# Kernel optimization log

Hardware: AMD Instinct MI355X
Metric: run time of the kernel (lower is better)

The kernel has to match this reference:

```python
import jax, jax.numpy as jnp
import numpy as np

B, T, F_DIM = 32, 512, 128
HID, OUT, KS = 256, 4, 3
PAD_LEN = 512          # round(T * (200/stage_timepoints - 1)), stage_timepoints = 100
MMD_SIGMA = 1.0
DILATIONS = (1, 2, 4)  # config.dilation_expand = 2, num_layers = 3


def setup_inputs() -> dict:
    key = jax.random.key(0)
    keys = iter(jax.random.split(key, 40))
    s = 0.05

    def lin(o, i):
        return jax.random.normal(next(keys), (o, i), jnp.float32) * s

    def vec(o):
        return jnp.zeros((o,), jnp.float32)

    inp = {
        "feature1": jax.random.normal(next(keys), (B, F_DIM, 1, T), jnp.float32),
        "feature2": jax.random.normal(next(keys), (B, F_DIM, 1, T), jnp.float32),
    }
    # cross-attention params (A and B branches)
    for tag in ("a", "b"):
        for nm in ("q", "k", "v"):
            inp["w%s_%s" % (nm, tag)] = lin(F_DIM, F_DIM)
            inp["b%s_%s" % (nm, tag)] = vec(F_DIM)
    # TCN layers
    in_ch = F_DIM
    for i in range(3):
        inp["conv_w%d" % i] = jax.random.normal(next(keys), (HID, in_ch, KS), jnp.float32) * s
        inp["conv_b%d" % i] = vec(HID)
        inp["res_w%d" % i] = lin(HID, in_ch)
        inp["res_b%d" % i] = vec(HID)
        in_ch = HID
    inp["fc_w"] = lin(OUT, HID)
    inp["fc_b"] = vec(OUT)
    return inp


def _cross_attention(A, Bseq, wq, bq, wk, bk, wv, bv):
    # A, Bseq: [B, T, F]
    Q = A @ wq.T + bq
    K = Bseq @ wk.T + bk
    V = Bseq @ wv.T + bv
    scale = 1.0 / jnp.sqrt(jnp.asarray(Q.shape[-1], Q.dtype))
    scores = jnp.einsum('btf,bsf->bts', Q, K) * scale
    w = jax.nn.softmax(scores, axis=-1)
    return jnp.einsum('bts,bsf->btf', w, V)


def _tcn_layer(x, cw, cb, rw, rb, dilation):
    # x: [B, C, T]; causal left pad then dilated conv
    pad = (KS - 1) * dilation
    xp = jnp.pad(x, ((0, 0), (0, 0), (pad, 0)))
    out = jax.lax.conv_general_dilated(
        xp, cw, window_strides=(1,), padding='VALID',
        rhs_dilation=(dilation,), dimension_numbers=('NCH', 'OIH', 'NCH'))
    out = jax.nn.relu(out + cb[None, :, None])
    res = jnp.einsum('bct,oc->bot', x, rw) + rb[None, :, None]
    return out + res


def _pairwise_dist(x, y):
    # x, y: [B, T, F] -> [B, B, T]; ||x_i - y_j||^2 per time point via norm expansion
    sx = jnp.sum(x * x, axis=-1)  # [B, T]
    sy = jnp.sum(y * y, axis=-1)  # [B, T]
    return sx[:, None, :] + sy[None, :, :] - 2.0 * jnp.einsum('itf,jtf->ijt', x, y)


def _mmd_loss(f1, f2):
    inv = 1.0 / (2.0 * MMD_SIGMA ** 2)
    K_XX = jnp.exp(-_pairwise_dist(f1, f1) * inv)
    K_YY = jnp.exp(-_pairwise_dist(f2, f2) * inv)
    K_XY = jnp.exp(-_pairwise_dist(f1, f2) * inv)
    return jnp.mean(K_XX + K_YY - 2.0 * K_XY)


def reference(feature1, feature2,
              wq_a, bq_a, wk_a, bk_a, wv_a, bv_a,
              wq_b, bq_b, wk_b, bk_b, wv_b, bv_b,
              conv_w0, conv_b0, res_w0, res_b0,
              conv_w1, conv_b1, res_w1, res_b1,
              conv_w2, conv_b2, res_w2, res_b2,
              fc_w, fc_b):
    # [B, F, 1, T] -> [B, T, F]
    f1 = jnp.transpose(feature1[:, :, 0, :], (0, 2, 1))
    f2 = jnp.transpose(feature2[:, :, 0, :], (0, 2, 1))

    f1 = _cross_attention(f2, f1, wq_a, bq_a, wk_a, bk_a, wv_a, bv_a) * f1 + f1
    f2 = _cross_attention(f1, f2, wq_b, bq_b, wk_b, bk_b, wv_b, bv_b) * f2 + f2

    # temporal-offset padding: f1 padded right, f2 padded left, then summed
    p1 = jnp.pad(f1, ((0, 0), (0, PAD_LEN), (0, 0)))
    p2 = jnp.pad(f2, ((0, 0), (PAD_LEN, 0), (0, 0)))
    x = jnp.transpose(p1 + p2, (0, 2, 1))  # [B, F, T+PAD]

    tcn_params = ((conv_w0, conv_b0, res_w0, res_b0),
                  (conv_w1, conv_b1, res_w1, res_b1),
                  (conv_w2, conv_b2, res_w2, res_b2))
    for (cw, cb, rw, rb), d in zip(tcn_params, DILATIONS):
        x = _tcn_layer(x, cw, cb, rw, rb, d)

    pooled = jnp.mean(x, axis=2)          # [B, HID]
    output = pooled @ fc_w.T + fc_b       # [B, OUT]
    loss = _mmd_loss(f1, f2)
    return output, loss
```

## Files before the change

kernel.cpp:

```cpp
#include <hip/hip_runtime.h>

#define BB 32
#define TT 512
#define FF 128
#define HID 256
#define TP 1024

typedef __attribute__((ext_vector_type(8))) short s16x8;
typedef __attribute__((ext_vector_type(8))) unsigned short u16x8;
typedef __attribute__((ext_vector_type(4))) unsigned short u16x4;
typedef __attribute__((ext_vector_type(4))) float f32x4;

static __device__ __forceinline__ unsigned short f2bf(float f) {
    unsigned u = __builtin_bit_cast(unsigned, f);
    u = (u + 0x7FFFu + ((u >> 16) & 1u)) >> 16;
    return (unsigned short)u;
}
static __device__ __forceinline__ float bf2f(unsigned short b) {
    return __builtin_bit_cast(float, ((unsigned)b) << 16);
}

static __device__ __forceinline__ void tcnw_prep(
    int idx, const float* __restrict__ cw, const float* __restrict__ rw,
    unsigned short* __restrict__ out, int Cin)
{
    int p = idx / (256 * Cin);
    int rem = idx - p * 256 * Cin;
    int o = rem / Cin, c = rem - o * Cin;
    float v = (p < 3) ? cw[(o * Cin + c) * 3 + p] : rw[o * Cin + c];
    out[idx] = f2bf(v);
}

__global__ __launch_bounds__(256) void prep_all_kernel(
    const float* __restrict__ wqa, const float* __restrict__ wka,
    const float* __restrict__ wva, const float* __restrict__ wqb,
    const float* __restrict__ wkb, const float* __restrict__ wvb,
    const float* __restrict__ cw0, const float* __restrict__ rw0,
    const float* __restrict__ cw1, const float* __restrict__ rw1,
    const float* __restrict__ cw2, const float* __restrict__ rw2,
    unsigned short* __restrict__ qkvw, unsigned short* __restrict__ wb0,
    unsigned short* __restrict__ wb1, unsigned short* __restrict__ wb2)
{
    int idx = blockIdx.x * 256 + threadIdx.x;
    if (idx < 98304) {
        int p = idx >> 14, rc = idx & 16383;
        const float* srcs[6] = {wqa, wka, wva, wqb, wkb, wvb};
        float v = srcs[p][rc];
        if (p == 0 || p == 3) v *= 0.088388347648318447f;
        qkvw[idx] = f2bf(v);
    } else if (idx < 229376) {
        tcnw_prep(idx - 98304, cw0, rw0, wb0, 128);
    } else if (idx < 491520) {
        tcnw_prep(idx - 229376, cw1, rw1, wb1, 256);
    } else if (idx < 753664) {
        tcnw_prep(idx - 491520, cw2, rw2, wb2, 256);
    }
}

__global__ __launch_bounds__(256) void proj_mfma_kernel(
    const void* __restrict__ xq_src, int xq_mode, long long xq_bs,
    const void* __restrict__ xkv_src, int xkv_mode, long long xkv_bs,
    const unsigned short* __restrict__ w3,
    const float* __restrict__ bq, const float* __restrict__ bk,
    const float* __restrict__ bv,
    unsigned short* __restrict__ Qo, unsigned short* __restrict__ Ko,
    unsigned short* __restrict__ Vt)
{
    int t0 = blockIdx.x * 32, b = blockIdx.y;
    __shared__ __align__(16) unsigned short xsq[32 * 136];
    __shared__ __align__(16) unsigned short xskv[32 * 136];
    int tid = threadIdx.x;
    int wid = tid >> 6, lane = tid & 63;
    int n = lane & 15, g = lane >> 4;
    int tsub = (wid & 1) * 16, fh = (wid >> 1) * 64;

    if (xq_mode == 0) {
        const float* s = (const float*)xq_src + (size_t)b * xq_bs;
        for (int l = tid; l < 4096; l += 256) {
            int c = l >> 5, tt = l & 31;
            xsq[tt * 136 + c] = f2bf(s[(size_t)c * TT + t0 + tt]);
        }
    } else {
        const unsigned short* s = (const unsigned short*)xq_src + (size_t)b * xq_bs;
        for (int l = tid; l < 512; l += 256) {
            int r = l >> 4, cc = l & 15;
            *(u16x8*)&xsq[r * 136 + cc * 8] = *(const u16x8*)&s[(size_t)(t0 + r) * FF + cc * 8];
        }
    }
    if (xkv_mode == 0) {
        const float* s = (const float*)xkv_src + (size_t)b * xkv_bs;
        for (int l = tid; l < 4096; l += 256) {
            int c = l >> 5, tt = l & 31;
            xskv[tt * 136 + c] = f2bf(s[(size_t)c * TT + t0 + tt]);
        }
    } else {
        const unsigned short* s = (const unsigned short*)xkv_src + (size_t)b * xkv_bs;
        for (int l = tid; l < 512; l += 256) {
            int r = l >> 4, cc = l & 15;
            *(u16x8*)&xskv[r * 136 + cc * 8] = *(const u16x8*)&s[(size_t)(t0 + r) * FF + cc * 8];
        }
    }
    __syncthreads();

    f32x4 acc[3][4];
#pragma unroll
    for (int p = 0; p < 3; ++p)
#pragma unroll
        for (int i = 0; i < 4; ++i) acc[p][i] = (f32x4){0.f, 0.f, 0.f, 0.f};

#pragma unroll
    for (int kk = 0; kk < 4; ++kk) {
        s16x8 bxq = *(const s16x8*)&xsq[(tsub + n) * 136 + kk * 32 + g * 8];
        s16x8 bxkv = *(const s16x8*)&xskv[(tsub + n) * 136 + kk * 32 + g * 8];
#pragma unroll
        for (int i = 0; i < 4; ++i) {
            const unsigned short* wb = &w3[(size_t)(fh + i * 16 + n) * 128 + kk * 32 + g * 8];
            s16x8 a0 = *(const s16x8*)&wb[0];
            s16x8 a1 = *(const s16x8*)&wb[16384];
            s16x8 a2 = *(const s16x8*)&wb[32768];
            acc[0][i] = __builtin_amdgcn_mfma_f32_16x16x32_bf16(a0, bxq, acc[0][i], 0, 0, 0);
            acc[1][i] = __builtin_amdgcn_mfma_f32_16x16x32_bf16(a1, bxkv, acc[1][i], 0, 0, 0);
            acc[2][i] = __builtin_amdgcn_mfma_f32_16x16x32_bf16(a2, bxkv, acc[2][i], 0, 0, 0);
        }
    }

    const float scale = 0.088388347648318447f;
    int t = t0 + tsub + n;
#pragma unroll
    for (int i = 0; i < 4; ++i) {
        int fb = fh + i * 16 + g * 4;
        u16x4 pk;
#pragma unroll
        for (int r = 0; r < 4; ++r) pk[r] = f2bf(acc[0][i][r] + bq[fb + r] * scale);
        *(u16x4*)&Qo[((size_t)b * TT + t) * FF + fb] = pk;
#pragma unroll
        for (int r = 0; r < 4; ++r) pk[r] = f2bf(acc[1][i][r] + bk[fb + r]);
        *(u16x4*)&Ko[((size_t)b * TT + t) * FF + fb] = pk;
#pragma unroll
        for (int r = 0; r < 4; ++r)
            Vt[((size_t)b * FF + fb + r) * TT + t] = f2bf(acc[2][i][r] + bv[fb + r]);
    }
}

__global__ __launch_bounds__(256) void attn_mfma_kernel(
    const unsigned short* __restrict__ Qb, const unsigned short* __restrict__ Kb,
    const unsigned short* __restrict__ Vtb,
    const float* __restrict__ orig, long long bso, int cso, int tso,
    float* __restrict__ out_tf, unsigned short* __restrict__ out_x, int xoff)
{
    __shared__ __align__(16) unsigned short Ks[64 * 136];
    __shared__ __align__(16) unsigned short Vs[128 * 72];
    __shared__ __align__(16) unsigned short Ps[4 * 16 * 68];

    int t0 = blockIdx.x * 64, b = blockIdx.y;
    int tid = threadIdx.x;
    int wid = tid >> 6, lane = tid & 63;
    int n = lane & 15, g = lane >> 4;
    int q0 = t0 + wid * 16;
    unsigned short* Pw = &Ps[wid * 1088];

    s16x8 qf[4];
#pragma unroll
    for (int kk = 0; kk < 4; ++kk)
        qf[kk] = *(const s16x8*)&Qb[((size_t)b * TT + q0 + n) * FF + kk * 32 + g * 8];

    u16x8 kst[4], vst[4];
#pragma unroll
    for (int ii = 0; ii < 4; ++ii) {
        int l = tid + 256 * ii;
        kst[ii] = *(const u16x8*)&Kb[((size_t)b * TT + (l >> 4)) * FF + (l & 15) * 8];
        vst[ii] = *(const u16x8*)&Vtb[((size_t)b * FF + (l >> 3)) * TT + (l & 7) * 8];
    }

    f32x4 O[8];
#pragma unroll
    for (int ft = 0; ft < 8; ++ft) O[ft] = (f32x4){0.f, 0.f, 0.f, 0.f};
    float m[4] = {-1e30f, -1e30f, -1e30f, -1e30f};
    float lsum[4] = {0.f, 0.f, 0.f, 0.f};

    for (int it = 0; it < 8; ++it) {
        __syncthreads();
#pragma unroll
        for (int ii = 0; ii < 4; ++ii) {
            int l = tid + 256 * ii;
            *(u16x8*)&Ks[(l >> 4) * 136 + (l & 15) * 8] = kst[ii];
            *(u16x8*)&Vs[(l >> 3) * 72 + (l & 7) * 8] = vst[ii];
        }
        __syncthreads();
        if (it < 7) {
            int s0n = (it + 1) * 64;
#pragma unroll
            for (int ii = 0; ii < 4; ++ii) {
                int l = tid + 256 * ii;
                kst[ii] = *(const u16x8*)&Kb[((size_t)b * TT + s0n + (l >> 4)) * FF + (l & 15) * 8];
                vst[ii] = *(const u16x8*)&Vtb[((size_t)b * FF + (l >> 3)) * TT + s0n + (l & 7) * 8];
            }
        }

        f32x4 acc[4];
#pragma unroll
        for (int st = 0; st < 4; ++st) acc[st] = (f32x4){0.f, 0.f, 0.f, 0.f};
        __builtin_amdgcn_s_setprio(1);
#pragma unroll
        for (int kk = 0; kk < 4; ++kk) {
#pragma unroll
            for (int st = 0; st < 4; ++st) {
                s16x8 kf = *(const s16x8*)&Ks[(st * 16 + n) * 136 + kk * 32 + g * 8];
                acc[st] = __builtin_amdgcn_mfma_f32_16x16x32_bf16(qf[kk], kf, acc[st], 0, 0, 0);
            }
        }
        __builtin_amdgcn_s_setprio(0);

        float mnew[4], c[4], rs[4];
#pragma unroll
        for (int r = 0; r < 4; ++r) {
            float tm = fmaxf(fmaxf(acc[0][r], acc[1][r]), fmaxf(acc[2][r], acc[3][r]));
#pragma unroll
            for (int msk = 1; msk < 16; msk <<= 1) tm = fmaxf(tm, __shfl_xor(tm, msk));
            mnew[r] = fmaxf(m[r], tm);
            c[r] = __expf(m[r] - mnew[r]);
            m[r] = mnew[r];
            rs[r] = 0.f;
        }
#pragma unroll
        for (int st = 0; st < 4; ++st) {
#pragma unroll
            for (int r = 0; r < 4; ++r) {
                float p = __expf(acc[st][r] - mnew[r]);
                rs[r] += p;
                Pw[(g * 4 + r) * 68 + st * 16 + n] = f2bf(p);
            }
        }
#pragma unroll
        for (int r = 0; r < 4; ++r) {
#pragma unroll
            for (int msk = 1; msk < 16; msk <<= 1) rs[r] += __shfl_xor(rs[r], msk);
            lsum[r] = lsum[r] * c[r] + rs[r];
        }
#pragma unroll
        for (int ft = 0; ft < 8; ++ft) {
#pragma unroll
            for (int r = 0; r < 4; ++r) O[ft][r] *= c[r];
        }

        __builtin_amdgcn_s_setprio(1);
#pragma unroll
        for (int ks = 0; ks < 2; ++ks) {
            s16x8 pf = *(const s16x8*)&Pw[n * 68 + ks * 32 + g * 8];
#pragma unroll
            for (int ft = 0; ft < 8; ++ft) {
                s16x8 vf = *(const s16x8*)&Vs[(ft * 16 + n) * 72 + ks * 32 + g * 8];
                O[ft] = __builtin_amdgcn_mfma_f32_16x16x32_bf16(pf, vf, O[ft], 0, 0, 0);
            }
        }
        __builtin_amdgcn_s_setprio(0);
    }

    float rinv[4];
#pragma unroll
    for (int r = 0; r < 4; ++r) rinv[r] = 1.f / lsum[r];
#pragma unroll
    for (int ft = 0; ft < 8; ++ft) {
        int f = ft * 16 + n;
#pragma unroll
        for (int r = 0; r < 4; ++r) {
            int q = q0 + g * 4 + r;
            float val = O[ft][r] * rinv[r];
            float xv = orig[bso * b + (size_t)f * cso + (size_t)q * tso];
            float res = val * xv + xv;
            out_tf[((size_t)b * TT + q) * FF + f] = res;
            out_x[((size_t)b * TP + xoff + q) * FF + f] = f2bf(res);
        }
    }
}

__global__ __launch_bounds__(256) void mmd_kernel(
    const float* __restrict__ f1, const float* __restrict__ f2,
    float* __restrict__ partials)
{
    int t = blockIdx.x;
    __shared__ __align__(16) unsigned short X1h[32 * 136], X1l[32 * 136];
    __shared__ __align__(16) unsigned short X2h[32 * 136], X2l[32 * 136];
    __shared__ float Gs[3][32][33];
    __shared__ float red[256];
    int tid = threadIdx.x;

    for (int l = tid; l < 4096; l += 256) {
        int i = l >> 7, f = l & 127;
        float v1 = f1[((size_t)i * TT + t) * FF + f];
        float v2 = f2[((size_t)i * TT + t) * FF + f];
        unsigned short h1 = f2bf(v1);
        unsigned short h2 = f2bf(v2);
        X1h[i * 136 + f] = h1;
        X1l[i * 136 + f] = f2bf(v1 - bf2f(h1));
        X2h[i * 136 + f] = h2;
        X2l[i * 136 + f] = f2bf(v2 - bf2f(h2));
    }
    __syncthreads();

    int wid = tid >> 6, lane = tid & 63;
    int n = lane & 15, g = lane >> 4;
#pragma unroll
    for (int uu = 0; uu < 3; ++uu) {
        int u = wid * 3 + uu;
        int gram = u >> 2, quad = u & 3;
        int qi = quad >> 1, qj = quad & 1;
        const unsigned short* Ah = (gram == 1) ? X2h : X1h;
        const unsigned short* Al = (gram == 1) ? X2l : X1l;
        const unsigned short* Bh = (gram == 0) ? X1h : X2h;
        const unsigned short* Bl = (gram == 0) ? X1l : X2l;
        f32x4 acc = (f32x4){0.f, 0.f, 0.f, 0.f};
#pragma unroll
        for (int kk = 0; kk < 4; ++kk) {
            int ao = (qi * 16 + n) * 136 + kk * 32 + g * 8;
            int bo = (qj * 16 + n) * 136 + kk * 32 + g * 8;
            s16x8 ah = *(const s16x8*)&Ah[ao];
            s16x8 al = *(const s16x8*)&Al[ao];
            s16x8 bh = *(const s16x8*)&Bh[bo];
            s16x8 bl = *(const s16x8*)&Bl[bo];
            acc = __builtin_amdgcn_mfma_f32_16x16x32_bf16(ah, bh, acc, 0, 0, 0);
            acc = __builtin_amdgcn_mfma_f32_16x16x32_bf16(ah, bl, acc, 0, 0, 0);
            acc = __builtin_amdgcn_mfma_f32_16x16x32_bf16(al, bh, acc, 0, 0, 0);
        }
#pragma unroll
        for (int r = 0; r < 4; ++r)
            Gs[gram][qi * 16 + g * 4 + r][qj * 16 + n] = acc[r];
    }
    __syncthreads();

    float s = 0.f;
#pragma unroll
    for (int r = 0; r < 4; ++r) {
        int p = tid + 256 * r;
        int i = p >> 5, j = p & 31;
        float d11 = Gs[0][i][i] + Gs[0][j][j] - 2.f * Gs[0][i][j];
        float d22 = Gs[1][i][i] + Gs[1][j][j] - 2.f * Gs[1][i][j];
        float d12 = Gs[0][i][i] + Gs[1][j][j] - 2.f * Gs[2][i][j];
        s += __expf(-0.5f * d11) + __expf(-0.5f * d22) - 2.f * __expf(-0.5f * d12);
    }
    red[tid] = s;
    __syncthreads();
    for (int off = 128; off; off >>= 1) {
        if (tid < off) red[tid] += red[tid + off];
        __syncthreads();
    }
    if (tid == 0) partials[t] = red[0];
}

__global__ __launch_bounds__(256, 2) void tcn_mfma_kernel(
    const unsigned short* __restrict__ x, int Cin, int d,
    const unsigned short* __restrict__ w4,
    const float* __restrict__ cb, const float* __restrict__ rb,
    unsigned short* __restrict__ out, float* __restrict__ pool_out, int do_pool)
{
    int t0 = blockIdx.x * 256, o0 = blockIdx.y * 64, b = blockIdx.z;
    __shared__ __align__(16) unsigned short smem[20800];
    __shared__ float pool_s[4][64];
    unsigned short* xs = smem;
    unsigned short* wsh = smem + 10560;
    int tid = threadIdx.x;
    int wid = tid >> 6, lane = tid & 63;
    int n = lane & 15, g = lane >> 4;
    int wt = wid * 64;
    int d2 = 2 * d;
    const unsigned short* xb = x + (size_t)b * TP * Cin;

    int gg = tid & 3;
    int xr0 = tid >> 2;
    int tg0 = t0 - d2 + xr0;
    bool xv4 = xr0 < d2;
    const unsigned short* wbase = w4 + (size_t)(o0 + (tid >> 2)) * Cin + gg * 8;
    size_t wps = (size_t)256 * Cin;

    u16x8 sx0, sx1, sx2, sx3, sx4, sw0, sw1, sw2, sw3;
    const u16x8 zz = {0, 0, 0, 0, 0, 0, 0, 0};
#define LDST(C0)                                                               \
    do {                                                                       \
        sx0 = (tg0 >= 0) ? *(const u16x8*)&xb[(size_t)tg0 * Cin + (C0) + gg * 8] : zz; \
        sx1 = *(const u16x8*)&xb[(size_t)(tg0 + 64) * Cin + (C0) + gg * 8];    \
        sx2 = *(const u16x8*)&xb[(size_t)(tg0 + 128) * Cin + (C0) + gg * 8];   \
        sx3 = *(const u16x8*)&xb[(size_t)(tg0 + 192) * Cin + (C0) + gg * 8];   \
        sx4 = xv4 ? *(const u16x8*)&xb[(size_t)(tg0 + 256) * Cin + (C0) + gg * 8] : zz; \
        sw0 = *(const u16x8*)&wbase[(C0)];                                     \
        sw1 = *(const u16x8*)&wbase[wps + (C0)];                               \
        sw2 = *(const u16x8*)&wbase[2 * wps + (C0)];                           \
        sw3 = *(const u16x8*)&wbase[3 * wps + (C0)];                           \
    } while (0)

    f32x4 accc[4][4], accr[4][4];
#pragma unroll
    for (int i = 0; i < 4; ++i)
#pragma unroll
        for (int j = 0; j < 4; ++j) {
            accc[i][j] = (f32x4){0.f, 0.f, 0.f, 0.f};
            accr[i][j] = (f32x4){0.f, 0.f, 0.f, 0.f};
        }

    LDST(0);
    for (int c0 = 0; c0 < Cin; c0 += 32) {
        __syncthreads();
        *(u16x8*)&xs[xr0 * 40 + gg * 8] = sx0;
        *(u16x8*)&xs[(xr0 + 64) * 40 + gg * 8] = sx1;
        *(u16x8*)&xs[(xr0 + 128) * 40 + gg * 8] = sx2;
        *(u16x8*)&xs[(xr0 + 192) * 40 + gg * 8] = sx3;
        if (xv4) *(u16x8*)&xs[(xr0 + 256) * 40 + gg * 8] = sx4;
        {
            int wrow = (tid >> 2) * 40 + gg * 8;
            *(u16x8*)&wsh[wrow] = sw0;
            *(u16x8*)&wsh[2560 + wrow] = sw1;
            *(u16x8*)&wsh[5120 + wrow] = sw2;
            *(u16x8*)&wsh[7680 + wrow] = sw3;
        }
        __syncthreads();
        if (c0 + 32 < Cin) LDST(c0 + 32);

        s16x8 bfr[4][3];
#pragma unroll
        for (int j = 0; j < 4; ++j) {
            int tl = wt + j * 16 + n;
#pragma unroll
            for (int k = 0; k < 3; ++k)
                bfr[j][k] = *(const s16x8*)&xs[(tl + k * d) * 40 + g * 8];
        }
        __builtin_amdgcn_s_setprio(1);
#pragma unroll
        for (int i = 0; i < 4; ++i) {
            int wrow = (i * 16 + n) * 40 + g * 8;
            s16x8 a0 = *(const s16x8*)&wsh[wrow];
            s16x8 a1 = *(const s16x8*)&wsh[2560 + wrow];
            s16x8 a2 = *(const s16x8*)&wsh[5120 + wrow];
            s16x8 ar = *(const s16x8*)&wsh[7680 + wrow];
#pragma unroll
            for (int j = 0; j < 4; ++j) {
                accc[i][j] = __builtin_amdgcn_mfma_f32_16x16x32_bf16(a0, bfr[j][0], accc[i][j], 0, 0, 0);
                accc[i][j] = __builtin_amdgcn_mfma_f32_16x16x32_bf16(a1, bfr[j][1], accc[i][j], 0, 0, 0);
                accc[i][j] = __builtin_amdgcn_mfma_f32_16x16x32_bf16(a2, bfr[j][2], accc[i][j], 0, 0, 0);
                accr[i][j] = __builtin_amdgcn_mfma_f32_16x16x32_bf16(ar, bfr[j][2], accr[i][j], 0, 0, 0);
            }
        }
        __builtin_amdgcn_s_setprio(0);
    }
#undef LDST

    if (!do_pool) {
        __syncthreads();
        unsigned short* ot = smem;
#pragma unroll
        for (int i = 0; i < 4; ++i) {
            int ob = o0 + i * 16 + g * 4;
            float cbv0 = cb[ob], cbv1 = cb[ob + 1], cbv2 = cb[ob + 2], cbv3 = cb[ob + 3];
            float rbv0 = rb[ob], rbv1 = rb[ob + 1], rbv2 = rb[ob + 2], rbv3 = rb[ob + 3];
#pragma unroll
            for (int j = 0; j < 4; ++j) {
                int tl = wt + j * 16 + n;
                u16x4 pk;
                pk[0] = f2bf(fmaxf(accc[i][j][0] + cbv0, 0.f) + accr[i][j][0] + rbv0);
                pk[1] = f2bf(fmaxf(accc[i][j][1] + cbv1, 0.f) + accr[i][j][1] + rbv1);
                pk[2] = f2bf(fmaxf(accc[i][j][2] + cbv2, 0.f) + accr[i][j][2] + rbv2);
                pk[3] = f2bf(fmaxf(accc[i][j][3] + cbv3, 0.f) + accr[i][j][3] + rbv3);
                *(u16x4*)&ot[tl * 66 + i * 16 + g * 4] = pk;
            }
        }
        __syncthreads();
        int tl = tid >> 3, c8 = tid & 7;
#pragma unroll
        for (int s = 0; s < 8; ++s) {
            int trow = tl + 32 * s;
            *(u16x8*)&out[((size_t)b * TP + t0 + trow) * HID + o0 + c8 * 8] =
                *(const u16x8*)&ot[trow * 66 + c8 * 8];
        }
    } else {
#pragma unroll
        for (int i = 0; i < 4; ++i) {
            int ob = o0 + i * 16 + g * 4;
            float cbv0 = cb[ob], cbv1 = cb[ob + 1], cbv2 = cb[ob + 2], cbv3 = cb[ob + 3];
            float rbv0 = rb[ob], rbv1 = rb[ob + 1], rbv2 = rb[ob + 2], rbv3 = rb[ob + 3];
            float ps0 = 0.f, ps1 = 0.f, ps2 = 0.f, ps3 = 0.f;
#pragma unroll
            for (int j = 0; j < 4; ++j) {
                ps0 += fmaxf(accc[i][j][0] + cbv0, 0.f) + accr[i][j][0] + rbv0;
                ps1 += fmaxf(accc[i][j][1] + cbv1, 0.f) + accr[i][j][1] + rbv1;
                ps2 += fmaxf(accc[i][j][2] + cbv2, 0.f) + accr[i][j][2] + rbv2;
                ps3 += fmaxf(accc[i][j][3] + cbv3, 0.f) + accr[i][j][3] + rbv3;
            }
#pragma unroll
            for (int msk = 1; msk < 16; msk <<= 1) {
                ps0 += __shfl_xor(ps0, msk);
                ps1 += __shfl_xor(ps1, msk);
                ps2 += __shfl_xor(ps2, msk);
                ps3 += __shfl_xor(ps3, msk);
            }
            if (n == 0) {
                int ol = i * 16 + g * 4;
                pool_s[wid][ol + 0] = ps0;
                pool_s[wid][ol + 1] = ps1;
                pool_s[wid][ol + 2] = ps2;
                pool_s[wid][ol + 3] = ps3;
            }
        }
        __syncthreads();
        if (tid < 64) {
            float s = pool_s[0][tid] + pool_s[1][tid] + pool_s[2][tid] + pool_s[3][tid];
            pool_out[((size_t)b * 4 + blockIdx.x) * HID + o0 + tid] = s;
        }
    }
}

__global__ __launch_bounds__(256) void final_kernel(
    const float* __restrict__ pp, const float* __restrict__ fcw,
    const float* __restrict__ fcb, const float* __restrict__ partials,
    float* __restrict__ dout)
{
    int tid = threadIdx.x;
    if (tid < 128) {
        int b = tid >> 2, k = tid & 3;
        float s = 0.f;
        for (int c = 0; c < HID; ++c) {
            float pc = 0.f;
#pragma unroll
            for (int xs = 0; xs < 4; ++xs) pc += pp[((size_t)b * 4 + xs) * HID + c];
            s += pc * fcw[k * HID + c];
        }
        dout[tid] = fcb[k] + s * (1.f / 1024.f);
    } else if (tid < 192) {
        int lane = tid - 128;
        float s = 0.f;
        for (int j = 0; j < 8; ++j) s += partials[lane + 64 * j];
        for (int off = 32; off; off >>= 1) s += __shfl_down(s, off);
        if (lane == 0) dout[128] = s * (1.f / (32.f * 32.f * 512.f));
    }
}

extern "C" void kernel_launch(void* const* d_in, const int* in_sizes, int n_in,
                              void* d_out, int out_size, void* d_ws, size_t ws_size,
                              hipStream_t stream)
{
    const float* feat1 = (const float*)d_in[0];
    const float* feat2 = (const float*)d_in[1];
    const float* wq_a = (const float*)d_in[2];
    const float* bq_a = (const float*)d_in[3];
    const float* wk_a = (const float*)d_in[4];
    const float* bk_a = (const float*)d_in[5];
    const float* wv_a = (const float*)d_in[6];
    const float* bv_a = (const float*)d_in[7];
    const float* wq_b = (const float*)d_in[8];
    const float* bq_b = (const float*)d_in[9];
    const float* wk_b = (const float*)d_in[10];
    const float* bk_b = (const float*)d_in[11];
    const float* wv_b = (const float*)d_in[12];
    const float* bv_b = (const float*)d_in[13];
    const float* cw0 = (const float*)d_in[14];
    const float* cb0 = (const float*)d_in[15];
    const float* rw0 = (const float*)d_in[16];
    const float* rb0 = (const float*)d_in[17];
    const float* cw1 = (const float*)d_in[18];
    const float* cb1 = (const float*)d_in[19];
    const float* rw1 = (const float*)d_in[20];
    const float* rb1 = (const float*)d_in[21];
    const float* cw2 = (const float*)d_in[22];
    const float* cb2 = (const float*)d_in[23];
    const float* rw2 = (const float*)d_in[24];
    const float* rb2 = (const float*)d_in[25];
    const float* fcw = (const float*)d_in[26];
    const float* fcb = (const float*)d_in[27];
    float* dout = (float*)d_out;

    float* ws = (float*)d_ws;
    unsigned short* Qbf = (unsigned short*)ws;
    unsigned short* Kbf = (unsigned short*)(ws + 1048576);
    unsigned short* Vt  = (unsigned short*)(ws + 2097152);
    float* f1tf = ws + 3145728;
    float* f2tf = ws + 5242880;
    unsigned short* xbuf = (unsigned short*)(ws + 7340032);
    unsigned short* wbuf = (unsigned short*)(ws + 9437184);
    unsigned short* wb0 = wbuf;
    unsigned short* wb1 = wbuf + 131072;
    unsigned short* wb2 = wbuf + 393216;
    unsigned short* qkvw = (unsigned short*)(ws + 9764864);
    unsigned short* w3a = qkvw;
    unsigned short* w3b = qkvw + 3 * 16384;
    float* poolpart = ws + 9814016;
    float* mmdpart  = ws + 9846784;
    unsigned short* h_a = (unsigned short*)ws;
    unsigned short* h_b = (unsigned short*)(ws + 4194304);

    prep_all_kernel<<<dim3(2944), 256, 0, stream>>>(
        wq_a, wk_a, wv_a, wq_b, wk_b, wv_b,
        cw0, rw0, cw1, rw1, cw2, rw2, qkvw, wb0, wb1, wb2);

    proj_mfma_kernel<<<dim3(16, 32), 256, 0, stream>>>(
        feat2, 0, 65536LL, feat1, 0, 65536LL, w3a,
        bq_a, bk_a, bv_a, Qbf, Kbf, Vt);
    attn_mfma_kernel<<<dim3(8, 32), 256, 0, stream>>>(
        Qbf, Kbf, Vt, feat1, 65536LL, 512, 1, f1tf, xbuf, 0);

    proj_mfma_kernel<<<dim3(16, 32), 256, 0, stream>>>(
        xbuf, 1, (long long)TP * FF, feat2, 0, 65536LL, w3b,
        bq_b, bk_b, bv_b, Qbf, Kbf, Vt);
    attn_mfma_kernel<<<dim3(8, 32), 256, 0, stream>>>(
        Qbf, Kbf, Vt, feat2, 65536LL, 512, 1, f2tf, xbuf, 512);

    mmd_kernel<<<dim3(512), 256, 0, stream>>>(f1tf, f2tf, mmdpart);

    tcn_mfma_kernel<<<dim3(4, 4, 32), 256, 0, stream>>>(xbuf, 128, 1, wb0, cb0, rb0, h_a, nullptr, 0);
    tcn_mfma_kernel<<<dim3(4, 4, 32), 256, 0, stream>>>(h_a, 256, 2, wb1, cb1, rb1, h_b, nullptr, 0);
    tcn_mfma_kernel<<<dim3(4, 4, 32), 256, 0, stream>>>(h_b, 256, 4, wb2, cb2, rb2, h_a, poolpart, 1);

    final_kernel<<<dim3(1), 256, 0, stream>>>(poolpart, fcw, fcb, mmdpart, dout);
}
```

Before: 180.3 us.

## Double-buffer TCN shared-memory stages and widen projection time tile

The TCN conv kernel now keeps two LDS stages for inputs and weights. It writes the next chunk into the spare buffer while computing on the current one, which cuts one of the two barriers per channel chunk and prefetches two chunks ahead. The weight tile row stride drops from 40 to 36 so both stages fit. Separately, the QKV projection kernel processes 64 timesteps per block instead of 32, reusing each weight fragment across two time tiles and halving the grid. Costs are higher LDS use, which may lower occupancy, more accumulator registers in proj, and possible bank conflicts from the new 36-element stride.

```diff
diff --git a/kernel.cpp b/kernel.cpp
--- a/kernel.cpp
+++ b/kernel.cpp
@@ -66,9 +66,9 @@
     unsigned short* __restrict__ Qo, unsigned short* __restrict__ Ko,
     unsigned short* __restrict__ Vt)
 {
-    int t0 = blockIdx.x * 32, b = blockIdx.y;
-    __shared__ __align__(16) unsigned short xsq[32 * 136];
-    __shared__ __align__(16) unsigned short xskv[32 * 136];
+    int t0 = blockIdx.x * 64, b = blockIdx.y;
+    __shared__ __align__(16) unsigned short xsq[64 * 136];
+    __shared__ __align__(16) unsigned short xskv[64 * 136];
     int tid = threadIdx.x;
     int wid = tid >> 6, lane = tid & 63;
     int n = lane & 15, g = lane >> 4;
@@ -76,69 +76,79 @@
 
     if (xq_mode == 0) {
         const float* s = (const float*)xq_src + (size_t)b * xq_bs;
-        for (int l = tid; l < 4096; l += 256) {
-            int c = l >> 5, tt = l & 31;
+        for (int l = tid; l < 8192; l += 256) {
+            int c = l >> 6, tt = l & 63;
             xsq[tt * 136 + c] = f2bf(s[(size_t)c * TT + t0 + tt]);
         }
     } else {
         const unsigned short* s = (const unsigned short*)xq_src + (size_t)b * xq_bs;
-        for (int l = tid; l < 512; l += 256) {
+        for (int l = tid; l < 1024; l += 256) {
             int r = l >> 4, cc = l & 15;
             *(u16x8*)&xsq[r * 136 + cc * 8] = *(const u16x8*)&s[(size_t)(t0 + r) * FF + cc * 8];
         }
     }
     if (xkv_mode == 0) {
         const float* s = (const float*)xkv_src + (size_t)b * xkv_bs;
-        for (int l = tid; l < 4096; l += 256) {
-            int c = l >> 5, tt = l & 31;
+        for (int l = tid; l < 8192; l += 256) {
+            int c = l >> 6, tt = l & 63;
             xskv[tt * 136 + c] = f2bf(s[(size_t)c * TT + t0 + tt]);
         }
     } else {
         const unsigned short* s = (const unsigned short*)xkv_src + (size_t)b * xkv_bs;
-        for (int l = tid; l < 512; l += 256) {
+        for (int l = tid; l < 1024; l += 256) {
             int r = l >> 4, cc = l & 15;
             *(u16x8*)&xskv[r * 136 + cc * 8] = *(const u16x8*)&s[(size_t)(t0 + r) * FF + cc * 8];
         }
     }
     __syncthreads();
 
-    f32x4 acc[3][4];
-#pragma unroll
-    for (int p = 0; p < 3; ++p)
-#pragma unroll
-        for (int i = 0; i < 4; ++i) acc[p][i] = (f32x4){0.f, 0.f, 0.f, 0.f};
+    f32x4 acc[2][3][4];
+#pragma unroll
+    for (int tt = 0; tt < 2; ++tt)
+#pragma unroll
+        for (int p = 0; p < 3; ++p)
+#pragma unroll
+            for (int i = 0; i < 4; ++i) acc[tt][p][i] = (f32x4){0.f, 0.f, 0.f, 0.f};
 
 #pragma unroll
     for (int kk = 0; kk < 4; ++kk) {
-        s16x8 bxq = *(const s16x8*)&xsq[(tsub + n) * 136 + kk * 32 + g * 8];
-        s16x8 bxkv = *(const s16x8*)&xskv[(tsub + n) * 136 + kk * 32 + g * 8];
+        s16x8 bxq0 = *(const s16x8*)&xsq[(tsub + n) * 136 + kk * 32 + g * 8];
+        s16x8 bxq1 = *(const s16x8*)&xsq[(32 + tsub + n) * 136 + kk * 32 + g * 8];
+        s16x8 bxk0 = *(const s16x8*)&xskv[(tsub + n) * 136 + kk * 32 + g * 8];
+        s16x8 bxk1 = *(const s16x8*)&xskv[(32 + tsub + n) * 136 + kk * 32 + g * 8];
 #pragma unroll
         for (int i = 0; i < 4; ++i) {
             const unsigned short* wb = &w3[(size_t)(fh + i * 16 + n) * 128 + kk * 32 + g * 8];
             s16x8 a0 = *(const s16x8*)&wb[0];
             s16x8 a1 = *(const s16x8*)&wb[16384];
             s16x8 a2 = *(const s16x8*)&wb[32768];
-            acc[0][i] = __builtin_amdgcn_mfma_f32_16x16x32_bf16(a0, bxq, acc[0][i], 0, 0, 0);
-            acc[1][i] = __builtin_amdgcn_mfma_f32_16x16x32_bf16(a1, bxkv, acc[1][i], 0, 0, 0);
-            acc[2][i] = __builtin_amdgcn_mfma_f32_16x16x32_bf16(a2, bxkv, acc[2][i], 0, 0, 0);
+            acc[0][0][i] = __builtin_amdgcn_mfma_f32_16x16x32_bf16(a0, bxq0, acc[0][0][i], 0, 0, 0);
+            acc[0][1][i] = __builtin_amdgcn_mfma_f32_16x16x32_bf16(a1, bxk0, acc[0][1][i], 0, 0, 0);
+            acc[0][2][i] = __builtin_amdgcn_mfma_f32_16x16x32_bf16(a2, bxk0, acc[0][2][i], 0, 0, 0);
+            acc[1][0][i] = __builtin_amdgcn_mfma_f32_16x16x32_bf16(a0, bxq1, acc[1][0][i], 0, 0, 0);
+            acc[1][1][i] = __builtin_amdgcn_mfma_f32_16x16x32_bf16(a1, bxk1, acc[1][1][i], 0, 0, 0);
+            acc[1][2][i] = __builtin_amdgcn_mfma_f32_16x16x32_bf16(a2, bxk1, acc[1][2][i], 0, 0, 0);
         }
     }
 
     const float scale = 0.088388347648318447f;
-    int t = t0 + tsub + n;
-#pragma unroll
-    for (int i = 0; i < 4; ++i) {
-        int fb = fh + i * 16 + g * 4;
-        u16x4 pk;
-#pragma unroll
-        for (int r = 0; r < 4; ++r) pk[r] = f2bf(acc[0][i][r] + bq[fb + r] * scale);
-        *(u16x4*)&Qo[((size_t)b * TT + t) * FF + fb] = pk;
-#pragma unroll
-        for (int r = 0; r < 4; ++r) pk[r] = f2bf(acc[1][i][r] + bk[fb + r]);
-        *(u16x4*)&Ko[((size_t)b * TT + t) * FF + fb] = pk;
-#pragma unroll
-        for (int r = 0; r < 4; ++r)
-            Vt[((size_t)b * FF + fb + r) * TT + t] = f2bf(acc[2][i][r] + bv[fb + r]);
+#pragma unroll
+    for (int tt = 0; tt < 2; ++tt) {
+        int t = t0 + tt * 32 + tsub + n;
+#pragma unroll
+        for (int i = 0; i < 4; ++i) {
+            int fb = fh + i * 16 + g * 4;
+            u16x4 pk;
+#pragma unroll
+            for (int r = 0; r < 4; ++r) pk[r] = f2bf(acc[tt][0][i][r] + bq[fb + r] * scale);
+            *(u16x4*)&Qo[((size_t)b * TT + t) * FF + fb] = pk;
+#pragma unroll
+            for (int r = 0; r < 4; ++r) pk[r] = f2bf(acc[tt][1][i][r] + bk[fb + r]);
+            *(u16x4*)&Ko[((size_t)b * TT + t) * FF + fb] = pk;
+#pragma unroll
+            for (int r = 0; r < 4; ++r)
+                Vt[((size_t)b * FF + fb + r) * TT + t] = f2bf(acc[tt][2][i][r] + bv[fb + r]);
+        }
     }
 }
 
@@ -354,10 +364,8 @@
     unsigned short* __restrict__ out, float* __restrict__ pool_out, int do_pool)
 {
     int t0 = blockIdx.x * 256, o0 = blockIdx.y * 64, b = blockIdx.z;
-    __shared__ __align__(16) unsigned short smem[20800];
+    __shared__ __align__(16) unsigned short smem[39552];
     __shared__ float pool_s[4][64];
-    unsigned short* xs = smem;
-    unsigned short* wsh = smem + 10560;
     int tid = threadIdx.x;
     int wid = tid >> 6, lane = tid & 63;
     int n = lane & 15, g = lane >> 4;
@@ -371,6 +379,8 @@
     bool xv4 = xr0 < d2;
     const unsigned short* wbase = w4 + (size_t)(o0 + (tid >> 2)) * Cin + gg * 8;
     size_t wps = (size_t)256 * Cin;
+    int xoff0 = xr0 * 40 + gg * 8;
+    int woff0 = (tid >> 2) * 36 + gg * 8;
 
     u16x8 sx0, sx1, sx2, sx3, sx4, sw0, sw1, sw2, sw3;
     const u16x8 zz = {0, 0, 0, 0, 0, 0, 0, 0};
@@ -386,6 +396,23 @@
         sw2 = *(const u16x8*)&wbase[2 * wps + (C0)];                           \
         sw3 = *(const u16x8*)&wbase[3 * wps + (C0)];                           \
     } while (0)
+#define WRSTAGE(XSW, WSW)                                                      \
+    do {                                                                       \
+        *(u16x8*)&(XSW)[xoff0] = sx0;                                          \
+        *(u16x8*)&(XSW)[xoff0 + 64 * 40] = sx1;                                \
+        *(u16x8*)&(XSW)[xoff0 + 128 * 40] = sx2;                               \
+        *(u16x8*)&(XSW)[xoff0 + 192 * 40] = sx3;                               \
+        if (xv4) *(u16x8*)&(XSW)[xoff0 + 256 * 40] = sx4;                      \
+        *(u16x8*)&(WSW)[woff0] = sw0;                                          \
+        *(u16x8*)&(WSW)[woff0 + 2304] = sw1;                                   \
+        *(u16x8*)&(WSW)[woff0 + 4608] = sw2;                                   \
+        *(u16x8*)&(WSW)[woff0 + 6912] = sw3;                                   \
+    } while (0)
+
+    unsigned short* xsr = smem;
+    unsigned short* xsw = smem + 10560;
+    unsigned short* wsr = smem + 21120;
+    unsigned short* wsw = smem + 30336;
 
     f32x4 accc[4][4], accr[4][4];
 #pragma unroll
@@ -397,22 +424,13 @@
         }
 
     LDST(0);
+    WRSTAGE(xsr, wsr);
+    if (Cin > 32) LDST(32);
+    __syncthreads();
+
     for (int c0 = 0; c0 < Cin; c0 += 32) {
-        __syncthreads();
-        *(u16x8*)&xs[xr0 * 40 + gg * 8] = sx0;
-        *(u16x8*)&xs[(xr0 + 64) * 40 + gg * 8] = sx1;
-        *(u16x8*)&xs[(xr0 + 128) * 40 + gg * 8] = sx2;
-        *(u16x8*)&xs[(xr0 + 192) * 40 + gg * 8] = sx3;
-        if (xv4) *(u16x8*)&xs[(xr0 + 256) * 40 + gg * 8] = sx4;
-        {
-            int wrow = (tid >> 2) * 40 + gg * 8;
-            *(u16x8*)&wsh[wrow] = sw0;
-            *(u16x8*)&wsh[2560 + wrow] = sw1;
-            *(u16x8*)&wsh[5120 + wrow] = sw2;
-            *(u16x8*)&wsh[7680 + wrow] = sw3;
-        }
-        __syncthreads();
-        if (c0 + 32 < Cin) LDST(c0 + 32);
+        if (c0 + 32 < Cin) WRSTAGE(xsw, wsw);
+        if (c0 + 64 < Cin) LDST(c0 + 64);
 
         s16x8 bfr[4][3];
 #pragma unroll
@@ -420,16 +438,16 @@
             int tl = wt + j * 16 + n;
 #pragma unroll
             for (int k = 0; k < 3; ++k)
-                bfr[j][k] = *(const s16x8*)&xs[(tl + k * d) * 40 + g * 8];
+                bfr[j][k] = *(const s16x8*)&xsr[(tl + k * d) * 40 + g * 8];
         }
         __builtin_amdgcn_s_setprio(1);
 #pragma unroll
         for (int i = 0; i < 4; ++i) {
-            int wrow = (i * 16 + n) * 40 + g * 8;
-            s16x8 a0 = *(const s16x8*)&wsh[wrow];
-            s16x8 a1 = *(const s16x8*)&wsh[2560 + wrow];
-            s16x8 a2 = *(const s16x8*)&wsh[5120 + wrow];
-            s16x8 ar = *(const s16x8*)&wsh[7680 + wrow];
+            int wrow = (i * 16 + n) * 36 + g * 8;
+            s16x8 a0 = *(const s16x8*)&wsr[wrow];
+            s16x8 a1 = *(const s16x8*)&wsr[2304 + wrow];
+            s16x8 a2 = *(const s16x8*)&wsr[4608 + wrow];
+            s16x8 ar = *(const s16x8*)&wsr[6912 + wrow];
 #pragma unroll
             for (int j = 0; j < 4; ++j) {
                 accc[i][j] = __builtin_amdgcn_mfma_f32_16x16x32_bf16(a0, bfr[j][0], accc[i][j], 0, 0, 0);
@@ -439,11 +457,15 @@
             }
         }
         __builtin_amdgcn_s_setprio(0);
+        __syncthreads();
+        unsigned short* tp;
+        tp = xsr; xsr = xsw; xsw = tp;
+        tp = wsr; wsr = wsw; wsw = tp;
     }
 #undef LDST
+#undef WRSTAGE
 
     if (!do_pool) {
-        __syncthreads();
         unsigned short* ot = smem;
 #pragma unroll
         for (int i = 0; i < 4; ++i) {
@@ -588,13 +610,13 @@
         wq_a, wk_a, wv_a, wq_b, wk_b, wv_b,
         cw0, rw0, cw1, rw1, cw2, rw2, qkvw, wb0, wb1, wb2);
 
-    proj_mfma_kernel<<<dim3(16, 32), 256, 0, stream>>>(
+    proj_mfma_kernel<<<dim3(8, 32), 256, 0, stream>>>(
         feat2, 0, 65536LL, feat1, 0, 65536LL, w3a,
         bq_a, bk_a, bv_a, Qbf, Kbf, Vt);
     attn_mfma_kernel<<<dim3(8, 32), 256, 0, stream>>>(
         Qbf, Kbf, Vt, feat1, 65536LL, 512, 1, f1tf, xbuf, 0);
 
-    proj_mfma_kernel<<<dim3(16, 32), 256, 0, stream>>>(
+    proj_mfma_kernel<<<dim3(8, 32), 256, 0, stream>>>(
         xbuf, 1, (long long)TP * FF, feat2, 0, 65536LL, w3b,
         bq_b, bk_b, bv_b, Qbf, Kbf, Vt);
     attn_mfma_kernel<<<dim3(8, 32), 256, 0, stream>>>(
```

Measured after the change: 232.9 us. +29.2%, slower.
